# Kernel optimization log

Hardware: AMD Instinct MI355X
Metric: run time of the kernel (lower is better)

## Reference

```python
import jax, jax.numpy as jnp
import numpy as np

EPS = 1e-6


def rms_norm(h, w):
    # T5-style: no mean subtraction, no bias; variance in fp32
    var = jnp.mean(jnp.square(h.astype(jnp.float32)), axis=-1, keepdims=True)
    h = h * jax.lax.rsqrt(var + EPS)
    return w * h


def split_heads(t, n_heads):
    b, n, d = t.shape
    return t.reshape(b, n, n_heads, d // n_heads).transpose(0, 2, 1, 3)  # [B,H,N,dk]


def unify_heads(t):
    b, h, n, dk = t.shape
    return t.transpose(0, 2, 1, 3).reshape(b, n, h * dk)


def attention(q_in, kv_in, bias, wq, wk, wv, wo, n_heads):
    q = split_heads(q_in @ wq, n_heads)   # [B,H,Nq,dk]
    k = split_heads(kv_in @ wk, n_heads)  # [B,H,Nk,dk]
    v = split_heads(kv_in @ wv, n_heads)
    scores = jnp.einsum('bhqd,bhkd->bhqk', q, k) + bias  # no 1/sqrt(dk) scaling (T5 style)
    w = jax.nn.softmax(scores.astype(jnp.float32), axis=-1).astype(scores.dtype)
    out = jnp.einsum('bhqk,bhkd->bhqd', w, v)
    return unify_heads(out) @ wo


def setup_inputs() -> dict:
    key = jax.random.key(0)
    ks = jax.random.split(key, 18)
    B, N, ENC_N, D, H, DFF = 4, 2048, 1024, 1024, 16, 4096
    s = 0.02
    inp = {
        'x': jax.random.normal(ks[0], (B, N, D), jnp.float32),
        'encoding': jax.random.normal(ks[1], (B, ENC_N, D), jnp.float32),
        'self_attention_position_bias': jax.random.normal(ks[2], (1, H, 1, N), jnp.float32),
        'enc_dec_attention_position_bias': jax.random.normal(ks[3], (1, H, N, ENC_N), jnp.float32),
        'wq_s': jax.random.normal(ks[4], (D, D), jnp.float32) * s,
        'wk_s': jax.random.normal(ks[5], (D, D), jnp.float32) * s,
        'wv_s': jax.random.normal(ks[6], (D, D), jnp.float32) * s,
        'wo_s': jax.random.normal(ks[7], (D, D), jnp.float32) * s,
        'wq_c': jax.random.normal(ks[8], (D, D), jnp.float32) * s,
        'wk_c': jax.random.normal(ks[9], (D, D), jnp.float32) * s,
        'wv_c': jax.random.normal(ks[10], (D, D), jnp.float32) * s,
        'wo_c': jax.random.normal(ks[11], (D, D), jnp.float32) * s,
        'ff1_w': jax.random.normal(ks[12], (D, DFF), jnp.float32) * s,
        'ff2_w': jax.random.normal(ks[13], (DFF, D), jnp.float32) * s,
        'norm1_w': jnp.ones((D,), jnp.float32),
        'norm2_w': jnp.ones((D,), jnp.float32),
        'norm3_w': jnp.ones((D,), jnp.float32),
    }
    return inp


def reference(x, encoding, self_attention_position_bias, enc_dec_attention_position_bias,
              wq_s, wk_s, wv_s, wo_s, wq_c, wk_c, wv_c, wo_c,
              ff1_w, ff2_w, norm1_w, norm2_w, norm3_w):
    n_heads = 16
    # --- self-attention (decoder: single query = last token) ---
    normed = rms_norm(x, norm1_w)
    q_in = normed[:, -1:, :]  # [B,1,D]
    attn_out = attention(q_in, normed, self_attention_position_bias,
                         wq_s, wk_s, wv_s, wo_s, n_heads)  # [B,1,D]
    x = x + attn_out  # broadcast over sequence, matching torch in-place broadcast
    # --- cross-attention ---
    normed = rms_norm(x, norm2_w)
    cross_out = attention(normed, encoding, enc_dec_attention_position_bias,
                          wq_c, wk_c, wv_c, wo_c, n_heads)  # [B,N,D]
    x = x + cross_out
    # --- MLP ---
    normed = rms_norm(x, norm3_w)
    mlp_out = jax.nn.relu(normed @ ff1_w) @ ff2_w
    return x + mlp_out
```

## Files before the change

### kernel.cpp

```cpp
#include <hip/hip_runtime.h>
#include <stdint.h>

typedef unsigned short bfu;
typedef __bf16 bf8v __attribute__((ext_vector_type(8)));
typedef unsigned short us8 __attribute__((ext_vector_type(8)));
typedef unsigned short us4 __attribute__((ext_vector_type(4)));
typedef float f4v __attribute__((ext_vector_type(4)));

__device__ __forceinline__ float bf2f(bfu u) {
    union { unsigned u; float f; } c; c.u = ((unsigned)u) << 16; return c.f;
}
__device__ __forceinline__ bfu f2bf(float f) {
    union { float f; unsigned u; } c; c.f = f;
    unsigned r = c.u + 0x7fffu + ((c.u >> 16) & 1u);
    return (bfu)(r >> 16);
}
__device__ __forceinline__ f4v mfma16(us8 a, us8 b, f4v c) {
    return __builtin_amdgcn_mfma_f32_16x16x32_bf16(
        __builtin_bit_cast(bf8v, a), __builtin_bit_cast(bf8v, b), c, 0, 0, 0);
}

template<int BM, int BN, int EPI>
__global__ __launch_bounds__(256) void gemm_bt(
    const bfu* __restrict__ A, const bfu* __restrict__ Bt,
    const float* __restrict__ resF, void* __restrict__ outP,
    int K, int lda, int ldb, int ldc,
    long long aZs, long long aBs, long long aHs,
    long long bZs, long long bBs, long long bHs,
    long long cZs, long long cBs, long long cHs,
    int bh0)
{
    constexpr int BK = 64;
    constexpr int WM = BM / 2, WN = BN / 2;
    constexpr int TM = WM / 16, TN = WN / 16;
    __shared__ __align__(16) bfu sA[BM * BK];
    __shared__ __align__(16) bfu sB[BN * BK];

    const int tid  = threadIdx.x;
    const int lane = tid & 63;
    const int wid  = tid >> 6;
    const int wr = wid >> 1, wc = wid & 1;

    const int z  = blockIdx.z;
    const int bh = bh0 + z;
    const int bb = bh >> 4, hh = bh & 15;
    const long long aOff = aZs * z + aBs * bb + aHs * hh;
    const long long bOff = bZs * z + bBs * bb + bHs * hh;
    const long long cOff = cZs * z + cBs * bb + cHs * hh;

    const int m0 = blockIdx.y * BM;
    const int n0 = blockIdx.x * BN;

    f4v acc[TM][TN];
    #pragma unroll
    for (int i = 0; i < TM; ++i)
        #pragma unroll
        for (int j = 0; j < TN; ++j)
            acc[i][j] = (f4v)0.0f;

    const bfu* gA = A + aOff + (long long)m0 * lda;
    const bfu* gB = Bt + bOff + (long long)n0 * ldb;
    const int rsub = tid >> 3;
    const int kb   = (tid & 7) * 8;

    for (int k0 = 0; k0 < K; k0 += BK) {
        us8 ra[BM / 32], rb[BN / 32];
        #pragma unroll
        for (int it = 0; it < BM / 32; ++it)
            ra[it] = *(const us8*)(gA + (long long)(it * 32 + rsub) * lda + k0 + kb);
        #pragma unroll
        for (int it = 0; it < BN / 32; ++it)
            rb[it] = *(const us8*)(gB + (long long)(it * 32 + rsub) * ldb + k0 + kb);

        __syncthreads();
        #pragma unroll
        for (int it = 0; it < BM / 32; ++it)
            *(us8*)&sA[(it * 32 + rsub) * BK + kb] = ra[it];
        #pragma unroll
        for (int it = 0; it < BN / 32; ++it)
            *(us8*)&sB[(it * 32 + rsub) * BK + kb] = rb[it];
        __syncthreads();

        #pragma unroll
        for (int kk = 0; kk < BK; kk += 32) {
            const int kro = kk + ((lane >> 4) << 3);
            us8 af[TM], bfr[TN];
            #pragma unroll
            for (int i = 0; i < TM; ++i)
                af[i] = *(const us8*)&sA[(wr * WM + i * 16 + (lane & 15)) * BK + kro];
            #pragma unroll
            for (int j = 0; j < TN; ++j)
                bfr[j] = *(const us8*)&sB[(wc * WN + j * 16 + (lane & 15)) * BK + kro];
            #pragma unroll
            for (int i = 0; i < TM; ++i)
                #pragma unroll
                for (int j = 0; j < TN; ++j)
                    acc[i][j] = mfma16(af[i], bfr[j], acc[i][j]);
        }
    }

    const int quad = lane >> 4;
    const int cn = lane & 15;
    #pragma unroll
    for (int i = 0; i < TM; ++i) {
        #pragma unroll
        for (int j = 0; j < TN; ++j) {
            const int col = n0 + wc * WN + j * 16 + cn;
            #pragma unroll
            for (int r = 0; r < 4; ++r) {
                const int row = m0 + wr * WM + i * 16 + quad * 4 + r;
                const long long idx = cOff + (long long)row * ldc + col;
                const float v = acc[i][j][r];
                if constexpr (EPI == 0) ((bfu*)outP)[idx] = f2bf(v);
                else if constexpr (EPI == 1) ((float*)outP)[idx] = resF[idx] + v;
                else ((bfu*)outP)[idx] = f2bf(fmaxf(v, 0.0f));
            }
        }
    }
}

#define SROW 1036
__global__ __launch_bounds__(256, 4) void xattn(
    const bfu* __restrict__ q2,
    const bfu* __restrict__ k2,
    const bfu* __restrict__ v2t,
    const float* __restrict__ bias,
    bfu* __restrict__ O)
{
    __shared__ __align__(16) bfu S[16 * SROW];
    const int tid = threadIdx.x, lane = tid & 63, wid = tid >> 6;
    const int quad = lane >> 4, l16 = lane & 15;
    const int bh = blockIdx.x;
    const int b = bh >> 4, h = bh & 15;
    const int q0 = blockIdx.y * 16;

    const float* bp = bias + ((long long)h * 2048 + q0 + wid * 4) * 1024 + lane * 16;
    f4v br0[4], br1[4];
    #pragma unroll
    for (int j = 0; j < 4; ++j) br0[j] = *(const f4v*)(bp + j * 4);
    #pragma unroll
    for (int j = 0; j < 4; ++j) br1[j] = *(const f4v*)(bp + 1024 + j * 4);

    const int kh0 = wid * 256;
    const bfu* qbase = q2 + ((long long)b * 2048 + q0) * 1024 + h * 64;
    const us8 af0 = *(const us8*)(qbase + (long long)l16 * 1024 + quad * 8);
    const us8 af1 = *(const us8*)(qbase + (long long)l16 * 1024 + 32 + quad * 8);
    const bfu* kbase = k2 + (long long)b * 1048576 + h * 64;
    #pragma unroll 4
    for (int t = 0; t < 16; ++t) {
        const int n0 = kh0 + t * 16;
        const bfu* kr = kbase + (long long)(n0 + l16) * 1024 + quad * 8;
        const us8 bf0 = *(const us8*)kr;
        const us8 bf1 = *(const us8*)(kr + 32);
        f4v acc = (f4v)0.0f;
        acc = mfma16(af0, bf0, acc);
        acc = mfma16(af1, bf1, acc);
        #pragma unroll
        for (int r = 0; r < 4; ++r)
            S[(quad * 4 + r) * SROW + n0 + l16] = f2bf(acc[r]);
    }
    f4v br2[4], br3[4];
    #pragma unroll
    for (int j = 0; j < 4; ++j) br2[j] = *(const f4v*)(bp + 2048 + j * 4);
    #pragma unroll
    for (int j = 0; j < 4; ++j) br3[j] = *(const f4v*)(bp + 3072 + j * 4);
    __syncthreads();

    auto dorow = [&](int row, const f4v bv[4]) {
        bfu* sp = &S[row * SROW + lane * 16];
        const us8 s0 = *(const us8*)sp;
        const us8 s1 = *(const us8*)(sp + 8);
        float v[16];
        #pragma unroll
        for (int j = 0; j < 8; ++j) v[j] = bf2f(s0[j]) + bv[j >> 2][j & 3];
        #pragma unroll
        for (int j = 0; j < 8; ++j) v[8 + j] = bf2f(s1[j]) + bv[2 + (j >> 2)][j & 3];
        float m = v[0];
        #pragma unroll
        for (int j = 1; j < 16; ++j) m = fmaxf(m, v[j]);
        #pragma unroll
        for (int o = 32; o; o >>= 1) m = fmaxf(m, __shfl_xor(m, o));
        float s = 0.f;
        #pragma unroll
        for (int j = 0; j < 16; ++j) { v[j] = __expf(v[j] - m); s += v[j]; }
        #pragma unroll
        for (int o = 32; o; o >>= 1) s += __shfl_xor(s, o);
        const float inv = 1.0f / s;
        us8 o0, o1;
        #pragma unroll
        for (int j = 0; j < 8; ++j) { o0[j] = f2bf(v[j] * inv); o1[j] = f2bf(v[8 + j] * inv); }
        *(us8*)sp = o0;
        *(us8*)(sp + 8) = o1;
    };
    dorow(wid * 4 + 0, br0);
    dorow(wid * 4 + 1, br1);
    dorow(wid * 4 + 2, br2);
    dorow(wid * 4 + 3, br3);
    __syncthreads();

    const bfu* vb = v2t + (long long)bh * 65536 + (long long)(wid * 16 + l16) * 1024;
    f4v a0 = (f4v)0.0f, a1 = (f4v)0.0f;
    for (int k0 = 0; k0 < 1024; k0 += 256) {
        us8 pa[8], vf[8];
        #pragma unroll
        for (int j = 0; j < 8; ++j) {
            pa[j] = *(const us8*)&S[l16 * SROW + k0 + j * 32 + quad * 8];
            vf[j] = *(const us8*)(vb + k0 + j * 32 + quad * 8);
        }
        #pragma unroll
        for (int j = 0; j < 8; j += 2) {
            a0 = mfma16(pa[j],     vf[j],     a0);
            a1 = mfma16(pa[j + 1], vf[j + 1], a1);
        }
    }
    const f4v acc3 = a0 + a1;
    bfu* ob = O + ((long long)b * 2048 + q0) * 1024 + h * 64 + wid * 16;
    #pragma unroll
    for (int r = 0; r < 4; ++r)
        ob[(long long)(quad * 4 + r) * 1024 + l16] = f2bf(acc3[r]);
}

__global__ __launch_bounds__(256) void cvt_f2b(
    const float* __restrict__ in, bfu* __restrict__ out)
{
    const long long i = ((long long)blockIdx.x * 256 + threadIdx.x) * 4;
    f4v v = *(const f4v*)(in + i);
    us4 o;
    #pragma unroll
    for (int k = 0; k < 4; ++k) o[k] = f2bf(v[k]);
    *(us4*)(out + i) = o;
}

__global__ __launch_bounds__(256) void transpose_plain(
    const float* __restrict__ in, bfu* __restrict__ out, int R, int C)
{
    __shared__ bfu t[32][33];
    const int r0 = blockIdx.y * 32, c0 = blockIdx.x * 32;
    const int tx = threadIdx.x, ty = threadIdx.y;
    #pragma unroll
    for (int i = 0; i < 32; i += 8)
        t[ty + i][tx] = f2bf(in[(long long)(r0 + ty + i) * C + c0 + tx]);
    __syncthreads();
    #pragma unroll
    for (int i = 0; i < 32; i += 8)
        out[(long long)(c0 + ty + i) * R + r0 + tx] = t[tx][ty + i];
}

__global__ __launch_bounds__(256) void transpose_w8(
    const float* p0, const float* p1, const float* p2, const float* p3,
    const float* p4, const float* p5, const float* p6, const float* p7,
    bfu* __restrict__ out)
{
    __shared__ bfu t[32][33];
    const float* srcs[8] = {p0, p1, p2, p3, p4, p5, p6, p7};
    const int zz = blockIdx.z;
    const float* in = srcs[zz];
    bfu* o = out + (long long)zz * 1048576;
    const int r0 = blockIdx.y * 32, c0 = blockIdx.x * 32;
    const int tx = threadIdx.x, ty = threadIdx.y;
    #pragma unroll
    for (int i = 0; i < 32; i += 8)
        t[ty + i][tx] = f2bf(in[(long long)(r0 + ty + i) * 1024 + c0 + tx]);
    __syncthreads();
    #pragma unroll
    for (int i = 0; i < 32; i += 8)
        o[(long long)(c0 + ty + i) * 1024 + r0 + tx] = t[tx][ty + i];
}

__global__ __launch_bounds__(256) void transpose_v2(
    const bfu* __restrict__ v2, bfu* __restrict__ v2t)
{
    __shared__ bfu t[32][33];
    const int z = blockIdx.z, b = z >> 4, h = z & 15;
    const bfu* in = v2 + (long long)b * 1048576 + h * 64;
    bfu* o = v2t + (long long)z * 65536;
    const int c0 = blockIdx.x * 32, r0 = blockIdx.y * 32;
    const int tx = threadIdx.x, ty = threadIdx.y;
    #pragma unroll
    for (int i = 0; i < 32; i += 8)
        t[ty + i][tx] = in[(long long)(r0 + ty + i) * 1024 + c0 + tx];
    __syncthreads();
    #pragma unroll
    for (int i = 0; i < 32; i += 8)
        o[(long long)(c0 + ty + i) * 1024 + r0 + tx] = t[tx][ty + i];
}

__device__ __forceinline__ float blockSum4(float v, float* red) {
    const int lane = threadIdx.x & 63, wid = threadIdx.x >> 6;
    #pragma unroll
    for (int o = 32; o; o >>= 1) v += __shfl_xor(v, o);
    if (lane == 0) red[wid] = v;
    __syncthreads();
    return red[0] + red[1] + red[2] + red[3];
}

__global__ __launch_bounds__(256) void rmsnorm_f32k(
    const float* __restrict__ X, const float* __restrict__ w, bfu* __restrict__ O)
{
    __shared__ float red[4];
    const long long row = blockIdx.x;
    const int tid = threadIdx.x;
    f4v xv = *(const f4v*)(X + row * 1024 + tid * 4);
    float ss = 0.f;
    #pragma unroll
    for (int i = 0; i < 4; ++i) ss += xv[i] * xv[i];
    ss = blockSum4(ss, red);
    const float sc = rsqrtf(ss * (1.0f / 1024.0f) + 1e-6f);
    f4v wv = *(const f4v*)(w + tid * 4);
    us4 o4;
    #pragma unroll
    for (int i = 0; i < 4; ++i) o4[i] = f2bf(xv[i] * sc * wv[i]);
    *(us4*)(O + row * 1024 + tid * 4) = o4;
}

__global__ __launch_bounds__(256) void add_bcast_rmsnorm(
    const float* __restrict__ X, const float* __restrict__ attn,
    const float* __restrict__ w, float* __restrict__ X1, bfu* __restrict__ O)
{
    __shared__ float red[4];
    const long long row = blockIdx.x;
    const int b = (int)(row >> 11);
    const int tid = threadIdx.x;
    f4v xv = *(const f4v*)(X + row * 1024 + tid * 4);
    f4v av = *(const f4v*)(attn + b * 1024 + tid * 4);
    f4v v;
    float ss = 0.f;
    #pragma unroll
    for (int i = 0; i < 4; ++i) { v[i] = xv[i] + av[i]; ss += v[i] * v[i]; }
    *(f4v*)(X1 + row * 1024 + tid * 4) = v;
    ss = blockSum4(ss, red);
    const float sc = rsqrtf(ss * (1.0f / 1024.0f) + 1e-6f);
    f4v wv = *(const f4v*)(w + tid * 4);
    us4 o4;
    #pragma unroll
    for (int i = 0; i < 4; ++i) o4[i] = f2bf(v[i] * sc * wv[i]);
    *(us4*)(O + row * 1024 + tid * 4) = o4;
}

template<int OUTF>
__global__ __launch_bounds__(256) void vecmat(
    const bfu* __restrict__ A, const bfu* __restrict__ Bt, void* __restrict__ out,
    int K, int N, long long aStride, long long aBase)
{
    __shared__ float sa[1024];
    const int tid = threadIdx.x;
    const int b = blockIdx.y;
    const bfu* ar = A + aBase + (long long)b * aStride;
    for (int k = tid; k < K; k += 256) sa[k] = bf2f(ar[k]);
    __syncthreads();
    const int n = blockIdx.x * 256 + tid;
    if (n < N) {
        const bfu* wr = Bt + (long long)n * K;
        float s = 0.f;
        for (int k = 0; k < K; k += 8) {
            us8 wv = *(const us8*)(wr + k);
            #pragma unroll
            for (int j = 0; j < 8; ++j) s += sa[k + j] * bf2f(wv[j]);
        }
        if constexpr (OUTF) ((float*)out)[(long long)b * N + n] = s;
        else ((bfu*)out)[(long long)b * N + n] = f2bf(s);
    }
}

__global__ __launch_bounds__(256) void decode_attn(
    const bfu* __restrict__ qs, const bfu* __restrict__ Kt,
    const bfu* __restrict__ Vt, const float* __restrict__ bias,
    bfu* __restrict__ osmall)
{
    const int bh = blockIdx.x, b = bh >> 4, h = bh & 15;
    const int tid = threadIdx.x, lane = tid & 63, wid = tid >> 6;
    __shared__ float sq[64];
    __shared__ float sc[2048];
    __shared__ float red[4];
    __shared__ float po[4][64];
    if (tid < 64) sq[tid] = bf2f(qs[b * 1024 + h * 64 + tid]);
    __syncthreads();

    const bfu* Kb = Kt + (long long)b * 2048 * 1024 + h * 64;
    float lmax = -1e30f;
    for (int k = tid; k < 2048; k += 256) {
        const us8* kr = (const us8*)(Kb + (long long)k * 1024);
        float s = 0.f;
        #pragma unroll
        for (int j = 0; j < 8; ++j) {
            us8 kv = kr[j];
            #pragma unroll
            for (int t = 0; t < 8; ++t) s += sq[j * 8 + t] * bf2f(kv[t]);
        }
        s += bias[h * 2048 + k];
        sc[k] = s;
        lmax = fmaxf(lmax, s);
    }
    #pragma unroll
    for (int o = 32; o; o >>= 1) lmax = fmaxf(lmax, __shfl_xor(lmax, o));
    if (lane == 0) red[wid] = lmax;
    __syncthreads();
    const float m = fmaxf(fmaxf(red[0], red[1]), fmaxf(red[2], red[3]));
    __syncthreads();

    float lsum = 0.f;
    for (int k = tid; k < 2048; k += 256) {
        const float e = __expf(sc[k] - m);
        sc[k] = e; lsum += e;
    }
    #pragma unroll
    for (int o = 32; o; o >>= 1) lsum += __shfl_xor(lsum, o);
    if (lane == 0) red[wid] = lsum;
    __syncthreads();
    const float S = red[0] + red[1] + red[2] + red[3];

    const bfu* Vb = Vt + (long long)b * 2048 * 1024 + h * 64;
    const int d = tid & 63, ks = tid >> 6;
    float a = 0.f;
    for (int k = ks * 512; k < ks * 512 + 512; ++k)
        a += sc[k] * bf2f(Vb[(long long)k * 1024 + d]);
    po[ks][d] = a;
    __syncthreads();
    if (tid < 64) {
        const float r = (po[0][tid] + po[1][tid] + po[2][tid] + po[3][tid]) / S;
        osmall[b * 1024 + h * 64 + tid] = f2bf(r);
    }
}

extern "C" void kernel_launch(void* const* d_in, const int* in_sizes, int n_in,
                              void* d_out, int out_size, void* d_ws, size_t ws_size,
                              hipStream_t stream) {
    (void)in_sizes; (void)n_in; (void)out_size; (void)ws_size;
    const float* x     = (const float*)d_in[0];
    const float* enc   = (const float*)d_in[1];
    const float* sbias = (const float*)d_in[2];
    const float* cbias = (const float*)d_in[3];
    const float* wq_s  = (const float*)d_in[4];
    const float* wk_s  = (const float*)d_in[5];
    const float* wv_s  = (const float*)d_in[6];
    const float* wo_s  = (const float*)d_in[7];
    const float* wq_c  = (const float*)d_in[8];
    const float* wk_c  = (const float*)d_in[9];
    const float* wv_c  = (const float*)d_in[10];
    const float* wo_c  = (const float*)d_in[11];
    const float* ff1   = (const float*)d_in[12];
    const float* ff2   = (const float*)d_in[13];
    const float* n1w   = (const float*)d_in[14];
    const float* n2w   = (const float*)d_in[15];
    const float* n3w   = (const float*)d_in[16];
    float* out = (float*)d_out;

    char* ws = (char*)d_ws;
    size_t off = 0;
    auto alloc = [&](size_t bytes) -> void* {
        void* p = (void*)(ws + off);
        off += (bytes + 255) & ~(size_t)255;
        return p;
    };
    bfu*   normed = (bfu*)alloc((size_t)8192 * 1024 * 2);
    bfu*   bufA   = (bfu*)alloc((size_t)8192 * 1024 * 2);
    bfu*   bufB   = (bfu*)alloc((size_t)8192 * 1024 * 2);
    bfu*   k2b    = (bfu*)alloc((size_t)4096 * 1024 * 2);
    bfu*   v2b    = (bfu*)alloc((size_t)4096 * 1024 * 2);
    bfu*   v2t    = (bfu*)alloc((size_t)4096 * 1024 * 2);
    bfu*   encb   = (bfu*)alloc((size_t)4096 * 1024 * 2);
    float* x1f    = (float*)alloc((size_t)8192 * 1024 * 4);
    bfu*   wT     = (bfu*)alloc((size_t)8 * 1048576 * 2);
    bfu*   ff1T   = (bfu*)alloc((size_t)4096 * 1024 * 2);
    bfu*   ff2T   = (bfu*)alloc((size_t)4096 * 1024 * 2);
    bfu*   qsb    = (bfu*)alloc(4 * 1024 * 2);
    bfu*   osm    = (bfu*)alloc(4 * 1024 * 2);
    float* attnv  = (float*)alloc(4 * 1024 * 4);
    bfu*   H1     = bufA;

    const dim3 tb32(32, 8);

    cvt_f2b<<<dim3(4096), 256, 0, stream>>>(enc, encb);
    transpose_w8<<<dim3(32, 32, 8), tb32, 0, stream>>>(
        wq_s, wk_s, wv_s, wo_s, wq_c, wk_c, wv_c, wo_c, wT);
    transpose_plain<<<dim3(128, 32, 1), tb32, 0, stream>>>(ff1, ff1T, 1024, 4096);
    transpose_plain<<<dim3(32, 128, 1), tb32, 0, stream>>>(ff2, ff2T, 4096, 1024);

    rmsnorm_f32k<<<dim3(8192), 256, 0, stream>>>(x, n1w, normed);

    gemm_bt<128, 128, 0><<<dim3(8, 64, 1), 256, 0, stream>>>(
        normed, wT + 1 * 1048576, nullptr, bufA, 1024, 1024, 1024, 1024,
        0, 0, 0, 0, 0, 0, 0, 0, 0, 0);
    gemm_bt<128, 128, 0><<<dim3(8, 64, 1), 256, 0, stream>>>(
        normed, wT + 2 * 1048576, nullptr, bufB, 1024, 1024, 1024, 1024,
        0, 0, 0, 0, 0, 0, 0, 0, 0, 0);
    vecmat<0><<<dim3(4, 4), 256, 0, stream>>>(normed, wT + 0 * 1048576, qsb,
        1024, 1024, (long long)2048 * 1024, (long long)2047 * 1024);
    decode_attn<<<dim3(64), 256, 0, stream>>>(qsb, bufA, bufB, sbias, osm);
    vecmat<1><<<dim3(4, 4), 256, 0, stream>>>(osm, wT + 3 * 1048576, attnv,
        1024, 1024, 1024, 0);
    add_bcast_rmsnorm<<<dim3(8192), 256, 0, stream>>>(x, attnv, n2w, x1f, normed);

    gemm_bt<128, 128, 0><<<dim3(8, 64, 1), 256, 0, stream>>>(
        normed, wT + 4 * 1048576, nullptr, bufA, 1024, 1024, 1024, 1024,
        0, 0, 0, 0, 0, 0, 0, 0, 0, 0);
    gemm_bt<128, 128, 0><<<dim3(8, 32, 1), 256, 0, stream>>>(
        encb, wT + 5 * 1048576, nullptr, k2b, 1024, 1024, 1024, 1024,
        0, 0, 0, 0, 0, 0, 0, 0, 0, 0);
    gemm_bt<128, 128, 0><<<dim3(8, 32, 1), 256, 0, stream>>>(
        encb, wT + 6 * 1048576, nullptr, v2b, 1024, 1024, 1024, 1024,
        0, 0, 0, 0, 0, 0, 0, 0, 0, 0);
    transpose_v2<<<dim3(2, 32, 64), tb32, 0, stream>>>(v2b, v2t);

    xattn<<<dim3(64, 128), 256, 0, stream>>>(bufA, k2b, v2t, cbias, bufB);

    gemm_bt<128, 128, 1><<<dim3(8, 64, 1), 256, 0, stream>>>(
        bufB, wT + 7 * 1048576, x1f, x1f, 1024, 1024, 1024, 1024,
        0, 0, 0, 0, 0, 0, 0, 0, 0, 0);

    rmsnorm_f32k<<<dim3(8192), 256, 0, stream>>>(x1f, n3w, normed);
    for (int mc = 0; mc < 8192; mc += 4096) {
        gemm_bt<128, 128, 2><<<dim3(32, 32, 1), 256, 0, stream>>>(
            normed + (long long)mc * 1024, ff1T, nullptr, H1,
            1024, 1024, 1024, 4096,
            0, 0, 0, 0, 0, 0, 0, 0, 0, 0);
        gemm_bt<128, 128, 1><<<dim3(8, 32, 1), 256, 0, stream>>>(
            H1, ff2T, x1f + (long long)mc * 1024, out + (long long)mc * 1024,
            4096, 4096, 4096, 1024,
            0, 0, 0, 0, 0, 0, 0, 0, 0, 0);
    }
}
```

Baseline: 1.127 ms.

## Fuse K/V projection GEMMs, shrink N=1024 tiles, and unchunk the MLP

New measurement: 1.106 ms. No clear change (-1.8%).

```diff
diff --git a/kernel.cpp b/kernel.cpp
--- a/kernel.cpp
+++ b/kernel.cpp
@@ -24,11 +24,7 @@
 __global__ __launch_bounds__(256) void gemm_bt(
     const bfu* __restrict__ A, const bfu* __restrict__ Bt,
     const float* __restrict__ resF, void* __restrict__ outP,
-    int K, int lda, int ldb, int ldc,
-    long long aZs, long long aBs, long long aHs,
-    long long bZs, long long bBs, long long bHs,
-    long long cZs, long long cBs, long long cHs,
-    int bh0)
+    int K, int lda, int ldb, int ldc)
 {
     constexpr int BK = 64;
     constexpr int WM = BM / 2, WN = BN / 2;
@@ -41,13 +37,6 @@
     const int wid  = tid >> 6;
     const int wr = wid >> 1, wc = wid & 1;
 
-    const int z  = blockIdx.z;
-    const int bh = bh0 + z;
-    const int bb = bh >> 4, hh = bh & 15;
-    const long long aOff = aZs * z + aBs * bb + aHs * hh;
-    const long long bOff = bZs * z + bBs * bb + bHs * hh;
-    const long long cOff = cZs * z + cBs * bb + cHs * hh;
-
     const int m0 = blockIdx.y * BM;
     const int n0 = blockIdx.x * BN;
 
@@ -58,8 +47,8 @@
         for (int j = 0; j < TN; ++j)
             acc[i][j] = (f4v)0.0f;
 
-    const bfu* gA = A + aOff + (long long)m0 * lda;
-    const bfu* gB = Bt + bOff + (long long)n0 * ldb;
+    const bfu* gA = A + (long long)m0 * lda;
+    const bfu* gB = Bt + (long long)n0 * ldb;
     const int rsub = tid >> 3;
     const int kb   = (tid & 7) * 8;
 
@@ -109,7 +98,7 @@
             #pragma unroll
             for (int r = 0; r < 4; ++r) {
                 const int row = m0 + wr * WM + i * 16 + quad * 4 + r;
-                const long long idx = cOff + (long long)row * ldc + col;
+                const long long idx = (long long)row * ldc + col;
                 const float v = acc[i][j][r];
                 if constexpr (EPI == 0) ((bfu*)outP)[idx] = f2bf(v);
                 else if constexpr (EPI == 1) ((float*)outP)[idx] = resF[idx] + v;
@@ -122,7 +111,7 @@
 #define SROW 1036
 __global__ __launch_bounds__(256, 4) void xattn(
     const bfu* __restrict__ q2,
-    const bfu* __restrict__ k2,
+    const bfu* __restrict__ kv2,
     const bfu* __restrict__ v2t,
     const float* __restrict__ bias,
     bfu* __restrict__ O)
@@ -145,11 +134,11 @@
     const bfu* qbase = q2 + ((long long)b * 2048 + q0) * 1024 + h * 64;
     const us8 af0 = *(const us8*)(qbase + (long long)l16 * 1024 + quad * 8);
     const us8 af1 = *(const us8*)(qbase + (long long)l16 * 1024 + 32 + quad * 8);
-    const bfu* kbase = k2 + (long long)b * 1048576 + h * 64;
+    const bfu* kbase = kv2 + (long long)b * 2097152 + h * 64;
     #pragma unroll 4
     for (int t = 0; t < 16; ++t) {
         const int n0 = kh0 + t * 16;
-        const bfu* kr = kbase + (long long)(n0 + l16) * 1024 + quad * 8;
+        const bfu* kr = kbase + (long long)(n0 + l16) * 2048 + quad * 8;
         const us8 bf0 = *(const us8*)kr;
         const us8 bf1 = *(const us8*)(kr + 32);
         f4v acc = (f4v)0.0f;
@@ -268,17 +257,17 @@
 }
 
 __global__ __launch_bounds__(256) void transpose_v2(
-    const bfu* __restrict__ v2, bfu* __restrict__ v2t)
+    const bfu* __restrict__ kv2, bfu* __restrict__ v2t)
 {
     __shared__ bfu t[32][33];
     const int z = blockIdx.z, b = z >> 4, h = z & 15;
-    const bfu* in = v2 + (long long)b * 1048576 + h * 64;
+    const bfu* in = kv2 + (long long)b * 2097152 + 1024 + h * 64;
     bfu* o = v2t + (long long)z * 65536;
     const int c0 = blockIdx.x * 32, r0 = blockIdx.y * 32;
     const int tx = threadIdx.x, ty = threadIdx.y;
     #pragma unroll
     for (int i = 0; i < 32; i += 8)
-        t[ty + i][tx] = in[(long long)(r0 + ty + i) * 1024 + c0 + tx];
+        t[ty + i][tx] = in[(long long)(r0 + ty + i) * 2048 + c0 + tx];
     __syncthreads();
     #pragma unroll
     for (int i = 0; i < 32; i += 8)
@@ -363,9 +352,8 @@
 }
 
 __global__ __launch_bounds__(256) void decode_attn(
-    const bfu* __restrict__ qs, const bfu* __restrict__ Kt,
-    const bfu* __restrict__ Vt, const float* __restrict__ bias,
-    bfu* __restrict__ osmall)
+    const bfu* __restrict__ qs, const bfu* __restrict__ KV,
+    const float* __restrict__ bias, bfu* __restrict__ osmall)
 {
     const int bh = blockIdx.x, b = bh >> 4, h = bh & 15;
     const int tid = threadIdx.x, lane = tid & 63, wid = tid >> 6;
@@ -376,10 +364,10 @@
     if (tid < 64) sq[tid] = bf2f(qs[b * 1024 + h * 64 + tid]);
     __syncthreads();
 
-    const bfu* Kb = Kt + (long long)b * 2048 * 1024 + h * 64;
+    const bfu* Kb = KV + (long long)b * 2048 * 2048 + h * 64;
     float lmax = -1e30f;
     for (int k = tid; k < 2048; k += 256) {
-        const us8* kr = (const us8*)(Kb + (long long)k * 1024);
+        const us8* kr = (const us8*)(Kb + (long long)k * 2048);
         float s = 0.f;
         #pragma unroll
         for (int j = 0; j < 8; ++j) {
@@ -409,11 +397,11 @@
     __syncthreads();
     const float S = red[0] + red[1] + red[2] + red[3];
 
-    const bfu* Vb = Vt + (long long)b * 2048 * 1024 + h * 64;
+    const bfu* Vb = KV + (long long)b * 2048 * 2048 + 1024 + h * 64;
     const int d = tid & 63, ks = tid >> 6;
     float a = 0.f;
     for (int k = ks * 512; k < ks * 512 + 512; ++k)
-        a += sc[k] * bf2f(Vb[(long long)k * 1024 + d]);
+        a += sc[k] * bf2f(Vb[(long long)k * 2048 + d]);
     po[ks][d] = a;
     __syncthreads();
     if (tid < 64) {
@@ -453,10 +441,8 @@
         return p;
     };
     bfu*   normed = (bfu*)alloc((size_t)8192 * 1024 * 2);
-    bfu*   bufA   = (bfu*)alloc((size_t)8192 * 1024 * 2);
-    bfu*   bufB   = (bfu*)alloc((size_t)8192 * 1024 * 2);
-    bfu*   k2b    = (bfu*)alloc((size_t)4096 * 1024 * 2);
-    bfu*   v2b    = (bfu*)alloc((size_t)4096 * 1024 * 2);
+    bfu*   kvs    = (bfu*)alloc((size_t)8192 * 2048 * 2);
+    bfu*   obuf   = (bfu*)alloc((size_t)8192 * 1024 * 2);
     bfu*   v2t    = (bfu*)alloc((size_t)4096 * 1024 * 2);
     bfu*   encb   = (bfu*)alloc((size_t)4096 * 1024 * 2);
     float* x1f    = (float*)alloc((size_t)8192 * 1024 * 4);
@@ -466,7 +452,9 @@
     bfu*   qsb    = (bfu*)alloc(4 * 1024 * 2);
     bfu*   osm    = (bfu*)alloc(4 * 1024 * 2);
     float* attnv  = (float*)alloc(4 * 1024 * 4);
-    bfu*   H1     = bufA;
+    bfu*   q2b = kvs;
+    bfu*   kv2 = kvs + (size_t)8192 * 1024;
+    bfu*   H1  = kvs;
 
     const dim3 tb32(32, 8);
 
@@ -478,45 +466,29 @@
 
     rmsnorm_f32k<<<dim3(8192), 256, 0, stream>>>(x, n1w, normed);
 
-    gemm_bt<128, 128, 0><<<dim3(8, 64, 1), 256, 0, stream>>>(
-        normed, wT + 1 * 1048576, nullptr, bufA, 1024, 1024, 1024, 1024,
-        0, 0, 0, 0, 0, 0, 0, 0, 0, 0);
-    gemm_bt<128, 128, 0><<<dim3(8, 64, 1), 256, 0, stream>>>(
-        normed, wT + 2 * 1048576, nullptr, bufB, 1024, 1024, 1024, 1024,
-        0, 0, 0, 0, 0, 0, 0, 0, 0, 0);
+    gemm_bt<128, 128, 0><<<dim3(16, 64), 256, 0, stream>>>(
+        normed, wT + 1 * 1048576, nullptr, kvs, 1024, 1024, 1024, 2048);
     vecmat<0><<<dim3(4, 4), 256, 0, stream>>>(normed, wT + 0 * 1048576, qsb,
         1024, 1024, (long long)2048 * 1024, (long long)2047 * 1024);
-    decode_attn<<<dim3(64), 256, 0, stream>>>(qsb, bufA, bufB, sbias, osm);
+    decode_attn<<<dim3(64), 256, 0, stream>>>(qsb, kvs, sbias, osm);
     vecmat<1><<<dim3(4, 4), 256, 0, stream>>>(osm, wT + 3 * 1048576, attnv,
         1024, 1024, 1024, 0);
     add_bcast_rmsnorm<<<dim3(8192), 256, 0, stream>>>(x, attnv, n2w, x1f, normed);
 
-    gemm_bt<128, 128, 0><<<dim3(8, 64, 1), 256, 0, stream>>>(
-        normed, wT + 4 * 1048576, nullptr, bufA, 1024, 1024, 1024, 1024,
-        0, 0, 0, 0, 0, 0, 0, 0, 0, 0);
-    gemm_bt<128, 128, 0><<<dim3(8, 32, 1), 256, 0, stream>>>(
-        encb, wT + 5 * 1048576, nullptr, k2b, 1024, 1024, 1024, 1024,
-        0, 0, 0, 0, 0, 0, 0, 0, 0, 0);
-    gemm_bt<128, 128, 0><<<dim3(8, 32, 1), 256, 0, stream>>>(
-        encb, wT + 6 * 1048576, nullptr, v2b, 1024, 1024, 1024, 1024,
-        0, 0, 0, 0, 0, 0, 0, 0, 0, 0);
-    transpose_v2<<<dim3(2, 32, 64), tb32, 0, stream>>>(v2b, v2t);
-
-    xattn<<<dim3(64, 128), 256, 0, stream>>>(bufA, k2b, v2t, cbias, bufB);
-
-    gemm_bt<128, 128, 1><<<dim3(8, 64, 1), 256, 0, stream>>>(
-        bufB, wT + 7 * 1048576, x1f, x1f, 1024, 1024, 1024, 1024,
-        0, 0, 0, 0, 0, 0, 0, 0, 0, 0);
+    gemm_bt<128, 64, 0><<<dim3(16, 64), 256, 0, stream>>>(
+        normed, wT + 4 * 1048576, nullptr, q2b, 1024, 1024, 1024, 1024);
+    gemm_bt<128, 64, 0><<<dim3(32, 32), 256, 0, stream>>>(
+        encb, wT + 5 * 1048576, nullptr, kv2, 1024, 1024, 1024, 2048);
+    transpose_v2<<<dim3(2, 32, 64), tb32, 0, stream>>>(kv2, v2t);
+
+    xattn<<<dim3(64, 128), 256, 0, stream>>>(q2b, kv2, v2t, cbias, obuf);
+
+    gemm_bt<128, 64, 1><<<dim3(16, 64), 256, 0, stream>>>(
+        obuf, wT + 7 * 1048576, x1f, x1f, 1024, 1024, 1024, 1024);
 
     rmsnorm_f32k<<<dim3(8192), 256, 0, stream>>>(x1f, n3w, normed);
-    for (int mc = 0; mc < 8192; mc += 4096) {
-        gemm_bt<128, 128, 2><<<dim3(32, 32, 1), 256, 0, stream>>>(
-            normed + (long long)mc * 1024, ff1T, nullptr, H1,
-            1024, 1024, 1024, 4096,
-            0, 0, 0, 0, 0, 0, 0, 0, 0, 0);
-        gemm_bt<128, 128, 1><<<dim3(8, 32, 1), 256, 0, stream>>>(
-            H1, ff2T, x1f + (long long)mc * 1024, out + (long long)mc * 1024,
-            4096, 4096, 4096, 1024,
-            0, 0, 0, 0, 0, 0, 0, 0, 0, 0);
-    }
-}
+    gemm_bt<128, 128, 2><<<dim3(32, 64), 256, 0, stream>>>(
+        normed, ff1T, nullptr, H1, 1024, 1024, 1024, 4096);
+    gemm_bt<128, 64, 1><<<dim3(16, 64), 256, 0, stream>>>(
+        H1, ff2T, x1f, out, 4096, 4096, 4096, 1024);
+}
```
